# Kernel tuning notes

Hardware: AMD Instinct MI355X
Metric: run time of the kernel (lower is better)

## Reference

```python
import jax, jax.numpy as jnp
import numpy as np

BN_EPS = 1e-5
SAMPLE_KEY = jax.random.key(42)


def setup_inputs() -> dict:
    key = jax.random.key(0)
    ks = jax.random.split(key, 12)
    B, W, E = 524288, 8, 4
    D = W * E  # 32, input dim of fc1

    def lin(k, fan_in, fan_out):
        k1, k2 = jax.random.split(k)
        bound = 1.0 / np.sqrt(fan_in)
        w = jax.random.uniform(k1, (fan_in, fan_out), jnp.float32, -bound, bound)
        b = jax.random.uniform(k2, (fan_out,), jnp.float32, -bound, bound)
        return w, b

    W1, b1 = lin(ks[0], D, 50)
    W2, b2 = lin(ks[1], 50, 30)
    W3, b3 = lin(ks[2], 30, 20)
    W4, b4 = lin(ks[3], 20, 15)
    W5, b5 = lin(ks[4], 15, W)
    # BatchNorm affine params (eval mode, running_mean=0, running_var=1)
    g1, be1 = jnp.ones((50,), jnp.float32), jnp.zeros((50,), jnp.float32)
    g2, be2 = jnp.ones((30,), jnp.float32), jnp.zeros((30,), jnp.float32)
    g3, be3 = jnp.ones((20,), jnp.float32), jnp.zeros((20,), jnp.float32)
    events = jax.random.normal(ks[5], (B, W, E), jnp.float32)
    return {"events": events,
            "W1": W1, "b1": b1, "g1": g1, "be1": be1,
            "W2": W2, "b2": b2, "g2": g2, "be2": be2,
            "W3": W3, "b3": b3, "g3": g3, "be3": be3,
            "W4": W4, "b4": b4, "W5": W5, "b5": b5}


def _bn_eval(x, g, b):
    # eval-mode BatchNorm1d with running_mean=0, running_var=1
    return x * (g / jnp.sqrt(1.0 + BN_EPS)) + b


def _probs(events, W1, b1, g1, be1, W2, b2, g2, be2, W3, b3, g3, be3, W4, b4, W5, b5):
    B = events.shape[0]
    x = events.reshape(B, -1)  # (B, window*event_size)
    h = jax.nn.relu(_bn_eval(x @ W1 + b1, g1, be1))
    h = jax.nn.relu(_bn_eval(h @ W2 + b2, g2, be2))
    h = jax.nn.relu(_bn_eval(h @ W3 + b3, g3, be3))
    h = jax.nn.relu(h @ W4 + b4)
    return jax.nn.sigmoid(h @ W5 + b5)  # (B, window_size)


def reference(events, W1, b1, g1, be1, W2, b2, g2, be2, W3, b3, g3, be3, W4, b4, W5, b5):
    p = _probs(events, W1, b1, g1, be1, W2, b2, g2, be2, W3, b3, g3, be3, W4, b4, W5, b5)
    # np.random.choice([0,1], p=[p, 1-p]) => P(choice=1) = 1 - p
    choice = jax.random.bernoulli(SAMPLE_KEY, 1.0 - p).astype(p.dtype)  # (B, W)
    chosen_events_np = 1.0 - choice
    flipped = jnp.abs(choice - p)            # prob of sampled outcome per element
    log_prob = jnp.log(jnp.prod(flipped, axis=1))  # (B,)
    return chosen_events_np, log_prob
```

## Files before the change

### kernel.cpp

```cpp
#include <hip/hip_runtime.h>
#include <math.h>

#define THREADS 256
#define TPW 8
#define ROWS_PER_BLOCK 512
#define P_MARGIN 2e-4f
#define FIXCAP 64

typedef float f32x4 __attribute__((ext_vector_type(4)));
typedef short short8 __attribute__((ext_vector_type(8)));
union Frag { unsigned u[4]; short8 s; };

#define FR1 0
#define FR2 2048
#define FR3 4096
#define FR4 5120
#define FR5 6144
#define VB1 6656
#define VS1 6708
#define VE1 6760
#define VB2 6812
#define VS2 6844
#define VE2 6876
#define VB3 6908
#define VS3 6928
#define VE3 6948
#define VB4 6968
#define VB5 6984
#define PZ  6992
#define WPOOL 7024

__device__ __forceinline__ void tf2x32(unsigned x0, unsigned x1,
                                       unsigned &o0, unsigned &o1) {
  const unsigned k0 = 0u;
  const unsigned k1 = 42u;
  const unsigned k2 = 0x1BD11BDAu ^ k0 ^ k1;
  x0 += k0; x1 += k1;
#define TF_R(r) { x0 += x1; x1 = (x1 << (r)) | (x1 >> (32 - (r))); x1 ^= x0; }
  TF_R(13) TF_R(15) TF_R(26) TF_R(6)
  x0 += k1; x1 += k2 + 1u;
  TF_R(17) TF_R(29) TF_R(16) TF_R(24)
  x0 += k2; x1 += k0 + 2u;
  TF_R(13) TF_R(15) TF_R(26) TF_R(6)
  x0 += k0; x1 += k1 + 3u;
  TF_R(17) TF_R(29) TF_R(16) TF_R(24)
  x0 += k1; x1 += k2 + 4u;
  TF_R(13) TF_R(15) TF_R(26) TF_R(6)
  x0 += k2; x1 += k0 + 5u;
#undef TF_R
  o0 = x0; o1 = x1;
}

__device__ __forceinline__ unsigned rtnb(float v) {
  unsigned b = __float_as_uint(v);
  return (b + 0x7FFFu + ((b >> 16) & 1u)) & 0xFFFF0000u;
}

__device__ __forceinline__ unsigned cvtpk(float a, float b) {
  unsigned r;
  asm("v_cvt_pk_bf16_f32 %0, %1, %2" : "=v"(r) : "v"(a), "v"(b));
  return r;
}

__device__ __forceinline__ void pack8(const float f[8], short8 &H, short8 &L) {
  Frag h, l;
#pragma unroll
  for (int d = 0; d < 4; ++d) {
    unsigned hd = cvtpk(f[2 * d], f[2 * d + 1]);
    h.u[d] = hd;
    float r0 = f[2 * d]     - __uint_as_float(hd << 16);
    float r1 = f[2 * d + 1] - __uint_as_float(hd & 0xFFFF0000u);
    l.u[d] = cvtpk(r0, r1);
  }
  H = h.s; L = l.s;
}

__device__ __forceinline__ f32x4 mfma16(short8 a, short8 b, f32x4 c) {
  return __builtin_amdgcn_mfma_f32_16x16x32_bf16(a, b, c, 0, 0, 0);
}

__device__ __forceinline__ short8 ldfrag(const float *sW, int dwoff) {
  return *reinterpret_cast<const short8 *>(sW + dwoff);
}
__device__ __forceinline__ f32x4 ldv4(const float *sW, int dwoff) {
  return *reinterpret_cast<const f32x4 *>(sW + dwoff);
}

template <int K, int N, int NT, int FB, bool PERM>
__device__ __forceinline__ void stageA(const float *__restrict__ W,
                                       float *sW, int t) {
  for (int i = t; i < K * N; i += THREADS) {
    int k = i / N, n = i - k * N;
    float v = W[i];
    unsigned hb = rtnb(v);
    unsigned lb = rtnb(v - __uint_as_float(hb));
    int kt = k >> 5, g = (k >> 3) & 3, e = k & 7, d = e >> 1, par = e & 1;
    int tile, r;
    if (PERM) {
      int pg = n >> 5, m = n & 31, tt = (m >> 2) & 1;
      r = ((m >> 3) << 2) | (m & 3);
      tile = pg * 2 + tt;
    } else {
      tile = n >> 4; r = n & 15;
    }
    int lane = g * 16 + r;
    int dwhi = FB + (kt * NT + tile) * 512 + lane * 4 + d;
    unsigned short *hp = reinterpret_cast<unsigned short *>(sW);
    hp[2 * dwhi + par] = (unsigned short)(hb >> 16);
    hp[2 * (dwhi + 256) + par] = (unsigned short)(lb >> 16);
  }
}

__device__ __forceinline__ void bnpack(f32x4 a0, f32x4 a1, const float *sW,
                                       int vs, int ve, int g,
                                       short8 &H, short8 &L) {
  f32x4 sc0 = ldv4(sW, vs + g * 8),     of0 = ldv4(sW, ve + g * 8);
  f32x4 sc1 = ldv4(sW, vs + g * 8 + 4), of1 = ldv4(sW, ve + g * 8 + 4);
  float f[8];
#pragma unroll
  for (int q = 0; q < 4; ++q) {
    f[q]     = fmaxf(fmaf(a0[q], sc0[q], of0[q]), 0.f);
    f[4 + q] = fmaxf(fmaf(a1[q], sc1[q], of1[q]), 0.f);
  }
  pack8(f, H, L);
}

__global__ __launch_bounds__(THREADS, 2)
void wtf_kernel(const float* __restrict__ events,
                const float* __restrict__ W1, const float* __restrict__ b1,
                const float* __restrict__ g1, const float* __restrict__ be1,
                const float* __restrict__ W2, const float* __restrict__ b2,
                const float* __restrict__ g2, const float* __restrict__ be2,
                const float* __restrict__ W3, const float* __restrict__ b3,
                const float* __restrict__ g3, const float* __restrict__ be3,
                const float* __restrict__ W4, const float* __restrict__ b4,
                const float* __restrict__ W5, const float* __restrict__ b5,
                float* __restrict__ out_chosen,
                float* __restrict__ out_logp,
                int B) {
  __shared__ float sW[WPOOL];
  __shared__ unsigned s_cnt;
  __shared__ unsigned s_rows[FIXCAP];
  __shared__ double sA[64];
  __shared__ double sB[64];
  __shared__ double sF[8];

  const int t = threadIdx.x;
  const float rden = (float)(1.0 / sqrt(1.0 + 1e-5));

  if (t == 0) s_cnt = 0;
  for (int i = t; i < WPOOL; i += THREADS) sW[i] = 0.f;
  __syncthreads();
  stageA<32, 50, 4, FR1, true>(W1, sW, t);
  stageA<50, 30, 2, FR2, true>(W2, sW, t);
  stageA<30, 20, 2, FR3, true>(W3, sW, t);
  stageA<20, 15, 2, FR4, true>(W4, sW, t);
  stageA<15,  8, 1, FR5, false>(W5, sW, t);
  if (t < 50)                  { sW[VB1 + t] = b1[t]; sW[VS1 + t] = g1[t] * rden; sW[VE1 + t] = be1[t]; }
  else if (t >= 64 && t < 94)  { int i = t - 64;  sW[VB2 + i] = b2[i]; sW[VS2 + i] = g2[i] * rden; sW[VE2 + i] = be2[i]; }
  else if (t >= 128 && t < 148){ int i = t - 128; sW[VB3 + i] = b3[i]; sW[VS3 + i] = g3[i] * rden; sW[VE3 + i] = be3[i]; }
  else if (t >= 192 && t < 207){ sW[VB4 + (t - 192)] = b4[t - 192]; }
  else if (t >= 224 && t < 232){ sW[VB5 + (t - 224)] = b5[t - 224]; }
  __syncthreads();

  const int w = t >> 6, lane = t & 63;
  const int c = lane & 15, g = lane >> 4;
  const int labase = lane * 4;

  const int wrow0 = blockIdx.x * ROWS_PER_BLOCK + w * (TPW * 16);
  const float4 *xp = reinterpret_cast<const float4 *>(
      events + (size_t)(wrow0 + c) * 32 + g * 8);
  float4 xA0 = xp[0], xA1 = xp[1], xB0 = xp[128], xB1 = xp[129];

#pragma unroll 1
  for (int it = 0; it < TPW / 2; ++it) {
    const int rA = wrow0 + it * 32;
    const int rB = rA + 16;

    short8 Xh[2], Xl[2];
    {
      float fA[8] = {xA0.x, xA0.y, xA0.z, xA0.w, xA1.x, xA1.y, xA1.z, xA1.w};
      float fB[8] = {xB0.x, xB0.y, xB0.z, xB0.w, xB1.x, xB1.y, xB1.z, xB1.w};
      pack8(fA, Xh[0], Xl[0]);
      pack8(fB, Xh[1], Xl[1]);
    }
    {
      const int nit = (it + 1 < TPW / 2) ? it + 1 : it;
      const int nx = nit * 256;
      xA0 = xp[nx]; xA1 = xp[nx + 1]; xB0 = xp[nx + 128]; xB1 = xp[nx + 129];
    }

    f32x4 a1[2][4];
#pragma unroll
    for (int ti = 0; ti < 4; ++ti) {
      short8 wh = ldfrag(sW, FR1 + ti * 512 + labase);
      short8 wl = ldfrag(sW, FR1 + ti * 512 + 256 + labase);
      f32x4 bias = ldv4(sW, VB1 + (ti >> 1) * 32 + g * 8 + (ti & 1) * 4);
#pragma unroll
      for (int u = 0; u < 2; ++u) {
        f32x4 acc = bias;
        acc = mfma16(wh, Xl[u], acc);
        acc = mfma16(wl, Xh[u], acc);
        a1[u][ti] = mfma16(wh, Xh[u], acc);
      }
    }

    short8 B2h[2][2], B2l[2][2];
#pragma unroll
    for (int u = 0; u < 2; ++u) {
      bnpack(a1[u][0], a1[u][1], sW, VS1,      VE1,      g, B2h[u][0], B2l[u][0]);
      bnpack(a1[u][2], a1[u][3], sW, VS1 + 32, VE1 + 32, g, B2h[u][1], B2l[u][1]);
    }

    f32x4 a2[2][2];
#pragma unroll
    for (int u = 0; u < 2; ++u) {
      f32x4 b0 = ldv4(sW, VB2 + g * 8);
      f32x4 b1v = ldv4(sW, VB2 + g * 8 + 4);
      a2[u][0] = b0; a2[u][1] = b1v;
    }
#pragma unroll
    for (int ti = 0; ti < 2; ++ti) {
#pragma unroll
      for (int kt = 0; kt < 2; ++kt) {
        short8 wh = ldfrag(sW, FR2 + (kt * 2 + ti) * 512 + labase);
        short8 wl = ldfrag(sW, FR2 + (kt * 2 + ti) * 512 + 256 + labase);
#pragma unroll
        for (int u = 0; u < 2; ++u) {
          a2[u][ti] = mfma16(wh, B2l[u][kt], a2[u][ti]);
          a2[u][ti] = mfma16(wl, B2h[u][kt], a2[u][ti]);
          a2[u][ti] = mfma16(wh, B2h[u][kt], a2[u][ti]);
        }
      }
    }

    short8 B3h[2], B3l[2];
#pragma unroll
    for (int u = 0; u < 2; ++u)
      bnpack(a2[u][0], a2[u][1], sW, VS2, VE2, g, B3h[u], B3l[u]);

    f32x4 a3[2][2];
#pragma unroll
    for (int ti = 0; ti < 2; ++ti) {
      short8 wh = ldfrag(sW, FR3 + ti * 512 + labase);
      short8 wl = ldfrag(sW, FR3 + ti * 512 + 256 + labase);
      f32x4 bias = ldv4(sW, VB3 + g * 8 + ti * 4);
#pragma unroll
      for (int u = 0; u < 2; ++u) {
        f32x4 acc = bias;
        acc = mfma16(wh, B3l[u], acc);
        acc = mfma16(wl, B3h[u], acc);
        a3[u][ti] = mfma16(wh, B3h[u], acc);
      }
    }

    short8 B4h[2], B4l[2];
#pragma unroll
    for (int u = 0; u < 2; ++u)
      bnpack(a3[u][0], a3[u][1], sW, VS3, VE3, g, B4h[u], B4l[u]);

    f32x4 a4[2][2];
#pragma unroll
    for (int ti = 0; ti < 2; ++ti) {
      short8 wh = ldfrag(sW, FR4 + ti * 512 + labase);
      short8 wl = ldfrag(sW, FR4 + ti * 512 + 256 + labase);
      f32x4 bias = ldv4(sW, VB4 + g * 8 + ti * 4);
#pragma unroll
      for (int u = 0; u < 2; ++u) {
        f32x4 acc = bias;
        acc = mfma16(wh, B4l[u], acc);
        acc = mfma16(wl, B4h[u], acc);
        a4[u][ti] = mfma16(wh, B4h[u], acc);
      }
    }

    short8 B5h[2], B5l[2];
#pragma unroll
    for (int u = 0; u < 2; ++u) {
      float f[8];
#pragma unroll
      for (int q = 0; q < 4; ++q) {
        f[q]     = fmaxf(a4[u][0][q], 0.f);
        f[4 + q] = fmaxf(a4[u][1][q], 0.f);
      }
      pack8(f, B5h[u], B5l[u]);
    }

    f32x4 a5[2];
    {
      short8 wh = ldfrag(sW, FR5 + labase);
      short8 wl = ldfrag(sW, FR5 + 256 + labase);
      f32x4 bias = ldv4(sW, VB5 + g * 4);
#pragma unroll
      for (int u = 0; u < 2; ++u) {
        f32x4 acc = bias;
        acc = mfma16(wh, B5l[u], acc);
        acc = mfma16(wl, B5h[u], acc);
        a5[u] = mfma16(wh, B5h[u], acc);
      }
    }

#pragma unroll
    for (int u = 0; u < 2; ++u) {
      const int row = (u ? rB : rA) + c;
      float s2v = __shfl_xor(a5[u][2], 32);
      float s3v = __shfl_xor(a5[u][3], 32);
      float l0 = (g < 2) ? a5[u][0] : s2v;
      float l1 = (g < 2) ? a5[u][1] : s3v;
      const int base = ((g & 1) << 2) | ((g >> 1) << 1);
      float p0 = 1.f / (1.f + __expf(-l0));
      float p1 = 1.f / (1.f + __expf(-l1));
      unsigned o0, o1, q0, q1;
      tf2x32(0u, 8u * (unsigned)row + (unsigned)base,      o0, o1);
      tf2x32(0u, 8u * (unsigned)row + (unsigned)base + 1u, q0, q1);
      float u0 = __uint_as_float(0x3F800000u | ((o0 ^ o1) >> 9)) - 1.f;
      float u1 = __uint_as_float(0x3F800000u | ((q0 ^ q1) >> 9)) - 1.f;
      float th0 = 1.f - p0, th1 = 1.f - p1;
      bool c0 = u0 < th0, c1 = u1 < th1;
      bool need = (fabsf(u0 - th0) < P_MARGIN) || (fabsf(u1 - th1) < P_MARGIN);
      float prod = (c0 ? th0 : p0) * (c1 ? th1 : p1);
      prod *= __shfl_xor(prod, 16);
      prod *= __shfl_xor(prod, 32);
      float2 chv = make_float2(c0 ? 0.f : 1.f, c1 ? 0.f : 1.f);
      *reinterpret_cast<float2 *>(out_chosen + (size_t)row * 8 + base) = chv;
      if (g == 0) out_logp[row] = __logf(prod);
      if (need) {
        unsigned i = atomicAdd(&s_cnt, 1u);
        if (i < FIXCAP) s_rows[i] = (unsigned)row;
      }
    }
  }

  __syncthreads();
  unsigned cnt = s_cnt;
  if (cnt > FIXCAP) cnt = FIXCAP;
  if (cnt == 0) return;

  const double denom = sqrt(1.0 + 1e-5);
  for (unsigned r = 0; r < cnt; ++r) {
    const int rb = (int)s_rows[r];

    if (t < 32) sA[t] = (double)events[(size_t)rb * 32 + t];
    __syncthreads();

    double v = 0.0;
    if (t < 50) {
#pragma unroll
      for (int k = 0; k < 32; ++k) v = fma(sA[k], (double)W1[k * 50 + t], v);
      v += (double)b1[t];
      v = v * ((double)g1[t] / denom) + (double)be1[t];
      v = v > 0.0 ? v : 0.0;
    }
    __syncthreads();
    if (t < 50) sB[t] = v;
    __syncthreads();

    v = 0.0;
    if (t < 30) {
#pragma unroll
      for (int k = 0; k < 50; ++k) v = fma(sB[k], (double)W2[k * 30 + t], v);
      v += (double)b2[t];
      v = v * ((double)g2[t] / denom) + (double)be2[t];
      v = v > 0.0 ? v : 0.0;
    }
    __syncthreads();
    if (t < 30) sA[t] = v;
    __syncthreads();

    v = 0.0;
    if (t < 20) {
#pragma unroll
      for (int k = 0; k < 30; ++k) v = fma(sA[k], (double)W3[k * 20 + t], v);
      v += (double)b3[t];
      v = v * ((double)g3[t] / denom) + (double)be3[t];
      v = v > 0.0 ? v : 0.0;
    }
    __syncthreads();
    if (t < 20) sB[t] = v;
    __syncthreads();

    v = 0.0;
    if (t < 15) {
#pragma unroll
      for (int k = 0; k < 20; ++k) v = fma(sB[k], (double)W4[k * 15 + t], v);
      v += (double)b4[t];
      v = v > 0.0 ? v : 0.0;
    }
    __syncthreads();
    if (t < 15) sA[t] = v;
    __syncthreads();

    if (t < 8) {
      v = 0.0;
#pragma unroll
      for (int k = 0; k < 15; ++k) v = fma(sA[k], (double)W5[k * 8 + t], v);
      v += (double)b5[t];
      double p = 1.0 / (1.0 + exp(-v));
      unsigned j = 8u * (unsigned)rb + (unsigned)t, o0, o1;
      tf2x32(0u, j, o0, o1);
      unsigned bits = o0 ^ o1;
      float u = __uint_as_float(0x3F800000u | (bits >> 9)) - 1.f;
      double thr = 1.0 - p;
      bool choice = ((double)u < thr);
      out_chosen[(size_t)rb * 8 + t] = choice ? 0.f : 1.f;
      sF[t] = choice ? thr : p;
    }
    __syncthreads();
    if (t == 0) {
      double prod = 1.0;
      for (int w2 = 0; w2 < 8; ++w2) prod *= sF[w2];
      out_logp[rb] = (float)log(prod);
    }
    __syncthreads();
  }
}

extern "C" void kernel_launch(void* const* d_in, const int* in_sizes, int n_in,
                              void* d_out, int out_size, void* d_ws, size_t ws_size,
                              hipStream_t stream) {
  const float* events = (const float*)d_in[0];
  const float* W1  = (const float*)d_in[1];
  const float* b1  = (const float*)d_in[2];
  const float* g1  = (const float*)d_in[3];
  const float* be1 = (const float*)d_in[4];
  const float* W2  = (const float*)d_in[5];
  const float* b2  = (const float*)d_in[6];
  const float* g2  = (const float*)d_in[7];
  const float* be2 = (const float*)d_in[8];
  const float* W3  = (const float*)d_in[9];
  const float* b3  = (const float*)d_in[10];
  const float* g3  = (const float*)d_in[11];
  const float* be3 = (const float*)d_in[12];
  const float* W4  = (const float*)d_in[13];
  const float* b4  = (const float*)d_in[14];
  const float* W5  = (const float*)d_in[15];
  const float* b5  = (const float*)d_in[16];

  const int B = in_sizes[0] / 32;
  float* out = (float*)d_out;
  float* out_chosen = out;
  float* out_logp   = out + (size_t)B * 8;

  const int blocks = (B + ROWS_PER_BLOCK - 1) / ROWS_PER_BLOCK;
  hipLaunchKernelGGL(wtf_kernel, dim3(blocks), dim3(THREADS), 0, stream,
                     events, W1, b1, g1, be1, W2, b2, g2, be2,
                     W3, b3, g3, be3, W4, b4, W5, b5,
                     out_chosen, out_logp, B);
}
```

Baseline: 225.6 us.

## Split fused MLP+sampling kernel into probability and sampling kernels

Splits the single fused kernel in two. The first runs the MFMA MLP and writes sigmoid probabilities into the chosen-output buffer with float4 stores. The second kernel uses one thread per row: it reads the probabilities back, runs the Threefry sampling, computes the log-probability and does the fp64 fix-up for rows near the threshold. The aim is to take the RNG and fix-up register pressure and divergence out of the MFMA kernel, but it adds a second launch and an extra round trip of B×8 floats through global memory. FIXCAP is also halved, which lowers per-block fix-up capacity and could drop needed fix-ups.

After: 234.6 us. +4.0%, slower.

```diff
diff --git a/kernel.cpp b/kernel.cpp
--- a/kernel.cpp
+++ b/kernel.cpp
@@ -5,7 +5,7 @@
 #define TPW 8
 #define ROWS_PER_BLOCK 512
 #define P_MARGIN 2e-4f
-#define FIXCAP 64
+#define FIXCAP 32
 
 typedef float f32x4 __attribute__((ext_vector_type(4)));
 typedef short short8 __attribute__((ext_vector_type(8)));
@@ -126,29 +126,21 @@
 }
 
 __global__ __launch_bounds__(THREADS, 2)
-void wtf_kernel(const float* __restrict__ events,
-                const float* __restrict__ W1, const float* __restrict__ b1,
-                const float* __restrict__ g1, const float* __restrict__ be1,
-                const float* __restrict__ W2, const float* __restrict__ b2,
-                const float* __restrict__ g2, const float* __restrict__ be2,
-                const float* __restrict__ W3, const float* __restrict__ b3,
-                const float* __restrict__ g3, const float* __restrict__ be3,
-                const float* __restrict__ W4, const float* __restrict__ b4,
-                const float* __restrict__ W5, const float* __restrict__ b5,
-                float* __restrict__ out_chosen,
-                float* __restrict__ out_logp,
-                int B) {
+void probs_kernel(const float* __restrict__ events,
+                  const float* __restrict__ W1, const float* __restrict__ b1,
+                  const float* __restrict__ g1, const float* __restrict__ be1,
+                  const float* __restrict__ W2, const float* __restrict__ b2,
+                  const float* __restrict__ g2, const float* __restrict__ be2,
+                  const float* __restrict__ W3, const float* __restrict__ b3,
+                  const float* __restrict__ g3, const float* __restrict__ be3,
+                  const float* __restrict__ W4, const float* __restrict__ b4,
+                  const float* __restrict__ W5, const float* __restrict__ b5,
+                  float* __restrict__ outP, int B) {
   __shared__ float sW[WPOOL];
-  __shared__ unsigned s_cnt;
-  __shared__ unsigned s_rows[FIXCAP];
-  __shared__ double sA[64];
-  __shared__ double sB[64];
-  __shared__ double sF[8];
 
   const int t = threadIdx.x;
   const float rden = (float)(1.0 / sqrt(1.0 + 1e-5));
 
-  if (t == 0) s_cnt = 0;
   for (int i = t; i < WPOOL; i += THREADS) sW[i] = 0.f;
   __syncthreads();
   stageA<32, 50, 4, FR1, true>(W1, sW, t);
@@ -215,9 +207,8 @@
     f32x4 a2[2][2];
 #pragma unroll
     for (int u = 0; u < 2; ++u) {
-      f32x4 b0 = ldv4(sW, VB2 + g * 8);
-      f32x4 b1v = ldv4(sW, VB2 + g * 8 + 4);
-      a2[u][0] = b0; a2[u][1] = b1v;
+      a2[u][0] = ldv4(sW, VB2 + g * 8);
+      a2[u][1] = ldv4(sW, VB2 + g * 8 + 4);
     }
 #pragma unroll
     for (int ti = 0; ti < 2; ++ti) {
@@ -300,35 +291,72 @@
       }
     }
 
-#pragma unroll
-    for (int u = 0; u < 2; ++u) {
-      const int row = (u ? rB : rA) + c;
-      float s2v = __shfl_xor(a5[u][2], 32);
-      float s3v = __shfl_xor(a5[u][3], 32);
-      float l0 = (g < 2) ? a5[u][0] : s2v;
-      float l1 = (g < 2) ? a5[u][1] : s3v;
-      const int base = ((g & 1) << 2) | ((g >> 1) << 1);
-      float p0 = 1.f / (1.f + __expf(-l0));
-      float p1 = 1.f / (1.f + __expf(-l1));
-      unsigned o0, o1, q0, q1;
-      tf2x32(0u, 8u * (unsigned)row + (unsigned)base,      o0, o1);
-      tf2x32(0u, 8u * (unsigned)row + (unsigned)base + 1u, q0, q1);
-      float u0 = __uint_as_float(0x3F800000u | ((o0 ^ o1) >> 9)) - 1.f;
-      float u1 = __uint_as_float(0x3F800000u | ((q0 ^ q1) >> 9)) - 1.f;
-      float th0 = 1.f - p0, th1 = 1.f - p1;
-      bool c0 = u0 < th0, c1 = u1 < th1;
-      bool need = (fabsf(u0 - th0) < P_MARGIN) || (fabsf(u1 - th1) < P_MARGIN);
-      float prod = (c0 ? th0 : p0) * (c1 ? th1 : p1);
-      prod *= __shfl_xor(prod, 16);
-      prod *= __shfl_xor(prod, 32);
-      float2 chv = make_float2(c0 ? 0.f : 1.f, c1 ? 0.f : 1.f);
-      *reinterpret_cast<float2 *>(out_chosen + (size_t)row * 8 + base) = chv;
-      if (g == 0) out_logp[row] = __logf(prod);
-      if (need) {
-        unsigned i = atomicAdd(&s_cnt, 1u);
-        if (i < FIXCAP) s_rows[i] = (unsigned)row;
-      }
-    }
+    {
+      f32x4 sw1;
+#pragma unroll
+      for (int q = 0; q < 4; ++q) sw1[q] = __shfl_xor(a5[1][q], 32);
+      f32x4 src = (g < 2) ? a5[0] : sw1;
+      const int row = ((g < 2) ? rA : rB) + c;
+      float4 pv;
+      pv.x = 1.f / (1.f + __expf(-src[0]));
+      pv.y = 1.f / (1.f + __expf(-src[1]));
+      pv.z = 1.f / (1.f + __expf(-src[2]));
+      pv.w = 1.f / (1.f + __expf(-src[3]));
+      *reinterpret_cast<float4 *>(outP + (size_t)row * 8 + (g & 1) * 4) = pv;
+    }
+  }
+}
+
+__global__ __launch_bounds__(THREADS, 4)
+void sample_kernel(const float* __restrict__ events,
+                   const float* __restrict__ W1, const float* __restrict__ b1,
+                   const float* __restrict__ g1, const float* __restrict__ be1,
+                   const float* __restrict__ W2, const float* __restrict__ b2,
+                   const float* __restrict__ g2, const float* __restrict__ be2,
+                   const float* __restrict__ W3, const float* __restrict__ b3,
+                   const float* __restrict__ g3, const float* __restrict__ be3,
+                   const float* __restrict__ W4, const float* __restrict__ b4,
+                   const float* __restrict__ W5, const float* __restrict__ b5,
+                   float* __restrict__ out_chosen,
+                   float* __restrict__ out_logp, int B) {
+  __shared__ unsigned s_cnt;
+  __shared__ unsigned s_rows[FIXCAP];
+  __shared__ double sA[64];
+  __shared__ double sB[64];
+  __shared__ double sF[8];
+
+  const int t = threadIdx.x;
+  if (t == 0) s_cnt = 0;
+  __syncthreads();
+
+  const int b = blockIdx.x * THREADS + t;
+  if (b < B) {
+    float4 *pc = reinterpret_cast<float4 *>(out_chosen + (size_t)b * 8);
+    float4 pv0 = pc[0], pv1 = pc[1];
+    float p[8] = {pv0.x, pv0.y, pv0.z, pv0.w, pv1.x, pv1.y, pv1.z, pv1.w};
+
+    bool need = false;
+    float prod = 1.f;
+    float ch[8];
+#pragma unroll
+    for (int w = 0; w < 8; ++w) {
+      unsigned j = 8u * (unsigned)b + (unsigned)w, o0, o1;
+      tf2x32(0u, j, o0, o1);
+      unsigned bits = o0 ^ o1;
+      float u = __uint_as_float(0x3F800000u | (bits >> 9)) - 1.f;
+      float thr = 1.f - p[w];
+      bool choice = u < thr;
+      need = need || (fabsf(u - thr) < P_MARGIN);
+      ch[w] = choice ? 0.f : 1.f;
+      prod *= choice ? thr : p[w];
+    }
+    if (need) {
+      unsigned i = atomicAdd(&s_cnt, 1u);
+      if (i < FIXCAP) s_rows[i] = (unsigned)b;
+    }
+    pc[0] = make_float4(ch[0], ch[1], ch[2], ch[3]);
+    pc[1] = make_float4(ch[4], ch[5], ch[6], ch[7]);
+    out_logp[b] = __logf(prod);
   }
 
   __syncthreads();
@@ -441,8 +469,14 @@
   float* out_chosen = out;
   float* out_logp   = out + (size_t)B * 8;
 
-  const int blocks = (B + ROWS_PER_BLOCK - 1) / ROWS_PER_BLOCK;
-  hipLaunchKernelGGL(wtf_kernel, dim3(blocks), dim3(THREADS), 0, stream,
+  const int blocks1 = (B + ROWS_PER_BLOCK - 1) / ROWS_PER_BLOCK;
+  hipLaunchKernelGGL(probs_kernel, dim3(blocks1), dim3(THREADS), 0, stream,
+                     events, W1, b1, g1, be1, W2, b2, g2, be2,
+                     W3, b3, g3, be3, W4, b4, W5, b5,
+                     out_chosen, B);
+
+  const int blocks2 = (B + THREADS - 1) / THREADS;
+  hipLaunchKernelGGL(sample_kernel, dim3(blocks2), dim3(THREADS), 0, stream,
                      events, W1, b1, g1, be1, W2, b2, g2, be2,
                      W3, b3, g3, be3, W4, b4, W5, b5,
                      out_chosen, out_logp, B);
```
